# Performance work log

Hardware: AMD Instinct MI355X
Metric: run time of the kernel (lower is better)

The kernel has to match this reference:

```python
import jax, jax.numpy as jnp
import numpy as np

B, S, D = 8, 1024, 1152
H = 16
HD = D // H
HID = int(D * 4.0)
LN_EPS = 1e-5


def layer_norm(x, w, b):
    m = jnp.mean(x, axis=-1, keepdims=True)
    v = jnp.mean(jnp.square(x - m), axis=-1, keepdims=True)
    return (x - m) * jax.lax.rsqrt(v + LN_EPS) * w + b


def modulate(x, shift, scale):
    # shift/scale: [B, D] broadcast over seq
    return x * (1.0 + scale[:, None, :]) + shift[:, None, :]


def setup_inputs() -> dict:
    key = jax.random.key(0)
    ks = jax.random.split(key, 16)
    s = 0.02
    return {
        "x": jax.random.normal(ks[0], (B, S, D), jnp.float32),
        "c": jax.random.normal(ks[1], (B, D), jnp.float32),
        "ln1_w": jnp.ones((D,), jnp.float32),
        "ln1_b": jnp.zeros((D,), jnp.float32),
        "wq": jax.random.normal(ks[2], (D, D), jnp.float32) * s,
        "wk": jax.random.normal(ks[3], (D, D), jnp.float32) * s,
        "wv": jax.random.normal(ks[4], (D, D), jnp.float32) * s,
        "wo": jax.random.normal(ks[5], (D, D), jnp.float32) * s,
        "wo_b": jnp.zeros((D,), jnp.float32),
        "ln2_w": jnp.ones((D,), jnp.float32),
        "ln2_b": jnp.zeros((D,), jnp.float32),
        "fc1_w": jax.random.normal(ks[6], (D, HID), jnp.float32) * s,
        "fc1_b": jnp.zeros((HID,), jnp.float32),
        "fc2_w": jax.random.normal(ks[7], (HID, D), jnp.float32) * s,
        "fc2_b": jnp.zeros((D,), jnp.float32),
        "ada_w": jax.random.normal(ks[8], (D, 6 * D), jnp.float32) * s,
        "ada_b": jnp.zeros((6 * D,), jnp.float32),
    }


def attention(x, wq, wk, wv, wo, wo_b):
    b, s, d = x.shape
    q = (x @ wq).reshape(b, s, H, HD).transpose(0, 2, 1, 3)  # [B,H,S,hd]
    k = (x @ wk).reshape(b, s, H, HD).transpose(0, 2, 1, 3)
    v = (x @ wv).reshape(b, s, H, HD).transpose(0, 2, 1, 3)
    scale = 1.0 / np.sqrt(HD).astype(np.float32)
    att = jnp.einsum("bhqd,bhkd->bhqk", q, k) * scale
    att = jax.nn.softmax(att, axis=-1)
    out = jnp.einsum("bhqk,bhkd->bhqd", att, v)
    out = out.transpose(0, 2, 1, 3).reshape(b, s, d)
    return out @ wo + wo_b


def reference(x, c, ln1_w, ln1_b, wq, wk, wv, wo, wo_b, ln2_w, ln2_b,
              fc1_w, fc1_b, fc2_w, fc2_b, ada_w, ada_b):
    mod = jax.nn.silu(c) @ ada_w + ada_b  # [B, 6D]
    sh_msa, sc_msa, g_msa, sh_mlp, sc_mlp, g_mlp = jnp.split(mod, 6, axis=1)
    h = modulate(layer_norm(x, ln1_w, ln1_b), sh_msa, sc_msa)
    x = x + g_msa[:, None, :] * attention(h, wq, wk, wv, wo, wo_b)
    h = modulate(layer_norm(x, ln2_w, ln2_b), sh_mlp, sc_mlp)
    h = jax.nn.gelu(h @ fc1_w + fc1_b, approximate=False) @ fc2_w + fc2_b
    x = x + g_mlp[:, None, :] * h
    return x
```

## Files before the change

kernel.cpp:

```cpp
#include <hip/hip_runtime.h>
#include <hip/hip_bf16.h>


typedef unsigned short u16;
typedef unsigned int u32;
typedef __attribute__((ext_vector_type(8))) short bf16x8;
typedef __attribute__((ext_vector_type(4))) float f32x4;
typedef __attribute__((ext_vector_type(16))) float f32x16;

#define MFMA16(a, b, c) __builtin_amdgcn_mfma_f32_16x16x32_bf16((a), (b), (c), 0, 0, 0)
#define MFMA32(a, b, c) __builtin_amdgcn_mfma_f32_32x32x16_bf16((a), (b), (c), 0, 0, 0)

__device__ __forceinline__ u16 f2bf(float f) {
  __hip_bfloat16 h = __float2bfloat16(f);
  return __builtin_bit_cast(u16, h);
}

__device__ __forceinline__ float bf2f(u16 u) {
  u32 v = ((u32)u) << 16;
  return __builtin_bit_cast(float, v);
}

__device__ __forceinline__ void gload16(const u16* g, u16* l) {
  __builtin_amdgcn_global_load_lds(
      (const __attribute__((address_space(1))) unsigned int*)(const void*)g,
      (__attribute__((address_space(3))) unsigned int*)(void*)l, 16, 0, 0);
}

__global__ __launch_bounds__(256) void k_modproj1(const float* __restrict__ cc,
                                                  const float* __restrict__ aw,
                                                  float* __restrict__ partial) {
  __shared__ float lc[8][144];
  int kc = blockIdx.y;
  for (int i = threadIdx.x; i < 1152; i += 256) {
    int b = i / 144, k = i % 144;
    float v = cc[b * 1152 + kc * 144 + k];
    lc[b][k] = v / (1.f + __expf(-v));
  }
  __syncthreads();
  int j = blockIdx.x * 256 + threadIdx.x;
  float acc[8] = {0, 0, 0, 0, 0, 0, 0, 0};
  for (int k = 0; k < 144; ++k) {
    float w = aw[(size_t)(kc * 144 + k) * 6912 + j];
    #pragma unroll
    for (int b = 0; b < 8; ++b) acc[b] += lc[b][k] * w;
  }
  #pragma unroll
  for (int b = 0; b < 8; ++b) partial[((size_t)kc * 8 + b) * 6912 + j] = acc[b];
}

__global__ __launch_bounds__(256) void k_modproj2(const float* __restrict__ partial,
                                                  const float* __restrict__ ab,
                                                  float* __restrict__ mo) {
  int j = blockIdx.x * 256 + threadIdx.x;
  float bias = ab[j];
  #pragma unroll
  for (int b = 0; b < 8; ++b) {
    float s = 0.f;
    #pragma unroll
    for (int kc = 0; kc < 8; ++kc) s += partial[((size_t)kc * 8 + b) * 6912 + j];
    mo[(size_t)b * 6912 + j] = s + bias;
  }
}

__global__ __launch_bounds__(256) void k_tcvt(const float* __restrict__ in, u16* __restrict__ out,
                                              int K, int N) {
  __shared__ float t[32][33];
  int tx = threadIdx.x & 31, ty = threadIdx.x >> 5;
  size_t bx = (size_t)blockIdx.x * 32, by = (size_t)blockIdx.y * 32;
  #pragma unroll
  for (int i = 0; i < 4; ++i) t[ty + 8 * i][tx] = in[(by + ty + 8 * i) * N + bx + tx];
  __syncthreads();
  #pragma unroll
  for (int i = 0; i < 4; ++i) out[(bx + ty + 8 * i) * K + by + tx] = f2bf(t[tx][ty + 8 * i]);
}

__global__ __launch_bounds__(256) void k_lnmod(const float* __restrict__ xin,
                                               const float* __restrict__ w,
                                               const float* __restrict__ bs,
                                               const float* __restrict__ mo,
                                               int sh_off, int sc_off, u16* __restrict__ o) {
  int row = blockIdx.x;
  int b = row >> 10;
  int tid = threadIdx.x;
  const float4* x4 = (const float4*)(xin + (size_t)row * 1152);
  float4 v0 = x4[tid];
  float4 v1 = make_float4(0.f, 0.f, 0.f, 0.f);
  if (tid < 32) v1 = x4[256 + tid];
  float s = v0.x + v0.y + v0.z + v0.w + v1.x + v1.y + v1.z + v1.w;
  float sq = v0.x * v0.x + v0.y * v0.y + v0.z * v0.z + v0.w * v0.w +
             v1.x * v1.x + v1.y * v1.y + v1.z * v1.z + v1.w * v1.w;
  #pragma unroll
  for (int d = 32; d > 0; d >>= 1) { s += __shfl_down(s, d); sq += __shfl_down(sq, d); }
  __shared__ float ps[4], pq[4];
  int wid = tid >> 6, lane = tid & 63;
  if (lane == 0) { ps[wid] = s; pq[wid] = sq; }
  __syncthreads();
  float S = ps[0] + ps[1] + ps[2] + ps[3];
  float SQ = pq[0] + pq[1] + pq[2] + pq[3];
  float mean = S * (1.f / 1152.f);
  float var = SQ * (1.f / 1152.f) - mean * mean;
  float rs = rsqrtf(var + 1e-5f);
  const float* shp = mo + (size_t)b * 6912 + sh_off;
  const float* scp = mo + (size_t)b * 6912 + sc_off;
  u16* orow = o + (size_t)row * 1152;
  {
    int col = 4 * tid;
    ushort4 u; float y;
    y = (v0.x - mean) * rs * w[col + 0] + bs[col + 0]; u.x = f2bf(y * (1.f + scp[col + 0]) + shp[col + 0]);
    y = (v0.y - mean) * rs * w[col + 1] + bs[col + 1]; u.y = f2bf(y * (1.f + scp[col + 1]) + shp[col + 1]);
    y = (v0.z - mean) * rs * w[col + 2] + bs[col + 2]; u.z = f2bf(y * (1.f + scp[col + 2]) + shp[col + 2]);
    y = (v0.w - mean) * rs * w[col + 3] + bs[col + 3]; u.w = f2bf(y * (1.f + scp[col + 3]) + shp[col + 3]);
    *(ushort4*)&orow[col] = u;
  }
  if (tid < 32) {
    int col = 1024 + 4 * tid;
    ushort4 u; float y;
    y = (v1.x - mean) * rs * w[col + 0] + bs[col + 0]; u.x = f2bf(y * (1.f + scp[col + 0]) + shp[col + 0]);
    y = (v1.y - mean) * rs * w[col + 1] + bs[col + 1]; u.y = f2bf(y * (1.f + scp[col + 1]) + shp[col + 1]);
    y = (v1.z - mean) * rs * w[col + 2] + bs[col + 2]; u.z = f2bf(y * (1.f + scp[col + 2]) + shp[col + 2]);
    y = (v1.w - mean) * rs * w[col + 3] + bs[col + 3]; u.w = f2bf(y * (1.f + scp[col + 3]) + shp[col + 3]);
    *(ushort4*)&orow[col] = u;
  }
}

template <int EPI>
__global__ __launch_bounds__(512, 2) void k_gemm8(const u16* __restrict__ A,
                                                  const u16* __restrict__ Bt,
                                                  int Kst, int klen,
                                                  u16* __restrict__ Cb,
                                                  const float* __restrict__ bias,
                                                  u16* __restrict__ vt) {
  const int tid = threadIdx.x;
  const int w = tid >> 6, lane = tid & 63;
  const int wm = w >> 2, wn = w & 3;
  const int l31 = lane & 31, hi = lane >> 5;

  const int nwg = gridDim.x * gridDim.y;
  const int id = blockIdx.y * gridDim.x + blockIdx.x;
  const int swz = (id & 7) * (nwg >> 3) + (id >> 3);
  const int tM = (swz / gridDim.x) * 256, tN = (swz % gridDim.x) * 256;
  const int koff = 0;

  __shared__ u16 lA[3][256 * 32];
  __shared__ u16 lB[3][256 * 32];
  f32x16 acc[4][2];
  #pragma unroll
  for (int m = 0; m < 4; ++m)
    #pragma unroll
    for (int n = 0; n < 2; ++n)
      #pragma unroll
      for (int r = 0; r < 16; ++r) acc[m][n][r] = 0.f;

  const int lrow = lane >> 2, lseg = lane & 3;
  const int fl = (lrow & 3) ^ ((lrow >> 2) & 3);
  const u16* gA = A + (size_t)(tM + w * 32 + lrow) * Kst + (lseg ^ fl) * 8 + koff;
  const u16* gB = Bt + (size_t)(tN + w * 32 + lrow) * Kst + (lseg ^ fl) * 8 + koff;
  const size_t rstep = (size_t)16 * Kst;
  const int wo0 = (w * 32) * 32, wo1 = (w * 32 + 16) * 32;
  const int fr = (l31 & 3) ^ ((l31 >> 2) & 3);
  const int c0 = (hi ^ fr) * 8;
  const int c1 = ((hi ^ fr) ^ 2) * 8;
  const int arow = (wm * 128 + l31) * 32;
  const int brow = (wn * 64 + l31) * 32;

#define STAGE(buf, ks)                        \
  do {                                        \
    gload16(gA + (ks), lA[buf] + wo0);        \
    gload16(gA + rstep + (ks), lA[buf] + wo1);\
    gload16(gB + (ks), lB[buf] + wo0);        \
    gload16(gB + rstep + (ks), lB[buf] + wo1);\
  } while (0)

#define COMPUTE(buf)                                                              \
  do {                                                                            \
    bf16x8 af[4][2], bf[2][2];                                                    \
    _Pragma("unroll")                                                             \
    for (int m = 0; m < 4; ++m) {                                                 \
      af[m][0] = *(const bf16x8*)&lA[buf][arow + m * 1024 + c0];                  \
      af[m][1] = *(const bf16x8*)&lA[buf][arow + m * 1024 + c1];                  \
    }                                                                             \
    _Pragma("unroll")                                                             \
    for (int n = 0; n < 2; ++n) {                                                 \
      bf[n][0] = *(const bf16x8*)&lB[buf][brow + n * 1024 + c0];                  \
      bf[n][1] = *(const bf16x8*)&lB[buf][brow + n * 1024 + c1];                  \
    }                                                                             \
    __builtin_amdgcn_s_setprio(1);                                                \
    _Pragma("unroll")                                                             \
    for (int m = 0; m < 4; ++m)                                                   \
      _Pragma("unroll")                                                           \
      for (int n = 0; n < 2; ++n) acc[m][n] = MFMA32(af[m][0], bf[n][0], acc[m][n]); \
    _Pragma("unroll")                                                             \
    for (int m = 0; m < 4; ++m)                                                   \
      _Pragma("unroll")                                                           \
      for (int n = 0; n < 2; ++n) acc[m][n] = MFMA32(af[m][1], bf[n][1], acc[m][n]); \
    __builtin_amdgcn_s_setprio(0);                                                \
  } while (0)

#define WAITBAR(Nst)                                          \
  do {                                                        \
    asm volatile("s_waitcnt vmcnt(" #Nst ")" ::: "memory");   \
    __builtin_amdgcn_s_barrier();                             \
    __builtin_amdgcn_sched_barrier(0);                        \
  } while (0)

  const int nt = klen >> 5;
  STAGE(0, 0);
  STAGE(1, 32);
  int ks = 64;
  for (int g = 0; g < nt / 3 - 1; ++g) {
    WAITBAR(4); STAGE(2, ks);      COMPUTE(0);
    WAITBAR(4); STAGE(0, ks + 32); COMPUTE(1);
    WAITBAR(4); STAGE(1, ks + 64); COMPUTE(2);
    ks += 96;
  }
  WAITBAR(4); STAGE(2, ks); COMPUTE(0);
  WAITBAR(4); COMPUTE(1);
  WAITBAR(0); COMPUTE(2);
#undef STAGE
#undef COMPUTE
#undef WAITBAR

  #pragma unroll
  for (int m = 0; m < 4; ++m)
    #pragma unroll
    for (int n = 0; n < 2; ++n) {
      int gcol = tN + wn * 64 + n * 32 + l31;
      #pragma unroll
      for (int q = 0; q < 4; ++q) {
        int grow0 = tM + wm * 128 + m * 32 + hi * 4 + q * 8;
        if (EPI == 3) {
          if (gcol < 2304) {
            #pragma unroll
            for (int r = 0; r < 4; ++r)
              Cb[(size_t)(grow0 + r) * 3456 + gcol] = f2bf(acc[m][n][q * 4 + r]);
          } else if (gcol < 3456) {
            int qq = gcol - 2304;
            int hh = qq / 72;
            int d = qq - hh * 72;
            int bb = grow0 >> 10, sl = grow0 & 1023;
            ushort4 u;
            u.x = f2bf(acc[m][n][q * 4 + 0]); u.y = f2bf(acc[m][n][q * 4 + 1]);
            u.z = f2bf(acc[m][n][q * 4 + 2]); u.w = f2bf(acc[m][n][q * 4 + 3]);
            *(ushort4*)&vt[(((size_t)bb * 16 + hh) * 72 + d) * 1024 + sl] = u;
          }
        } else {
          const int NC = gridDim.x * 256;
          float bi = bias[gcol];
          #pragma unroll
          for (int r = 0; r < 4; ++r) {
            float z = acc[m][n][q * 4 + r] + bi;
            float z2 = z * z;
            float u = z * __fmaf_rn(z2, -0.0713548162f, -1.5957691216f);
            float e = __expf(u);
            Cb[(size_t)(grow0 + r) * NC + gcol] = f2bf(z * __builtin_amdgcn_rcpf(1.f + e));
          }
        }
      }
    }
}

template <int EPI>
__global__ __launch_bounds__(256) void k_gemm(const u16* __restrict__ A, const u16* __restrict__ Bt,
                                              int Kst, int klen, u16* __restrict__ Cb,
                                              float* __restrict__ Cf,
                                              const float* __restrict__ bias,
                                              const float* __restrict__ res,
                                              const float* __restrict__ mo, int goff,
                                              u16* __restrict__ vt) {
  const int tid = threadIdx.x;
  const int w = tid >> 6, lane = tid & 63;
  const int wr = w >> 1, wc = w & 1;
  const int l31 = lane & 31, hi = lane >> 5;

  const int nwg = gridDim.x * gridDim.y;
  const int id = blockIdx.y * gridDim.x + blockIdx.x;
  const int swz = (id & 7) * (nwg >> 3) + (id >> 3);
  const int tM = (swz / gridDim.x) * 128, tN = (swz % gridDim.x) * 128;
  const int N = gridDim.x * 128;
  const int koff = blockIdx.z * klen;

  __shared__ u16 lA[3][128 * 32];
  __shared__ u16 lB[3][128 * 32];
  f32x16 acc[2][2];
  #pragma unroll
  for (int m = 0; m < 2; ++m)
    #pragma unroll
    for (int n = 0; n < 2; ++n)
      #pragma unroll
      for (int r = 0; r < 16; ++r) acc[m][n][r] = 0.f;

  const int lrow = lane >> 2, lseg = lane & 3;
  const int fl = (lrow & 3) ^ ((lrow >> 2) & 3);
  const u16* gA = A + (size_t)(tM + w * 32 + lrow) * Kst + (lseg ^ fl) * 8 + koff;
  const u16* gB = Bt + (size_t)(tN + w * 32 + lrow) * Kst + (lseg ^ fl) * 8 + koff;
  const size_t rstep = (size_t)16 * Kst;
  const int wo0 = (w * 32) * 32, wo1 = (w * 32 + 16) * 32;
  const int fr = (l31 & 3) ^ ((l31 >> 2) & 3);
  const int c0 = (hi ^ fr) * 8;
  const int c1 = ((hi ^ fr) ^ 2) * 8;
  const int arow = (wr * 64 + l31) * 32;
  const int brow = (wc * 64 + l31) * 32;

#define STAGE(buf, ks)                        \
  do {                                        \
    gload16(gA + (ks), lA[buf] + wo0);        \
    gload16(gA + rstep + (ks), lA[buf] + wo1);\
    gload16(gB + (ks), lB[buf] + wo0);        \
    gload16(gB + rstep + (ks), lB[buf] + wo1);\
  } while (0)

#define COMPUTE(buf)                                                            \
  do {                                                                          \
    bf16x8 a00 = *(const bf16x8*)&lA[buf][arow + c0];                           \
    bf16x8 a01 = *(const bf16x8*)&lA[buf][arow + c1];                           \
    bf16x8 a10 = *(const bf16x8*)&lA[buf][arow + 1024 + c0];                    \
    bf16x8 a11 = *(const bf16x8*)&lA[buf][arow + 1024 + c1];                    \
    bf16x8 b00 = *(const bf16x8*)&lB[buf][brow + c0];                           \
    bf16x8 b01 = *(const bf16x8*)&lB[buf][brow + c1];                           \
    bf16x8 b10 = *(const bf16x8*)&lB[buf][brow + 1024 + c0];                    \
    bf16x8 b11 = *(const bf16x8*)&lB[buf][brow + 1024 + c1];                    \
    __builtin_amdgcn_s_setprio(1);                                              \
    acc[0][0] = MFMA32(a00, b00, acc[0][0]);                                    \
    acc[0][1] = MFMA32(a00, b10, acc[0][1]);                                    \
    acc[1][0] = MFMA32(a10, b00, acc[1][0]);                                    \
    acc[1][1] = MFMA32(a10, b10, acc[1][1]);                                    \
    acc[0][0] = MFMA32(a01, b01, acc[0][0]);                                    \
    acc[0][1] = MFMA32(a01, b11, acc[0][1]);                                    \
    acc[1][0] = MFMA32(a11, b01, acc[1][0]);                                    \
    acc[1][1] = MFMA32(a11, b11, acc[1][1]);                                    \
    __builtin_amdgcn_s_setprio(0);                                              \
  } while (0)

#define WAITBAR(Nst)                                          \
  do {                                                        \
    asm volatile("s_waitcnt vmcnt(" #Nst ")" ::: "memory");   \
    __builtin_amdgcn_s_barrier();                             \
    __builtin_amdgcn_sched_barrier(0);                        \
  } while (0)

  const int nt = klen >> 5;
  STAGE(0, 0);
  STAGE(1, 32);
  int ks = 64;
  for (int g = 0; g < nt / 3 - 1; ++g) {
    WAITBAR(4); STAGE(2, ks);      COMPUTE(0);
    WAITBAR(4); STAGE(0, ks + 32); COMPUTE(1);
    WAITBAR(4); STAGE(1, ks + 64); COMPUTE(2);
    ks += 96;
  }
  WAITBAR(4); STAGE(2, ks); COMPUTE(0);
  WAITBAR(4); COMPUTE(1);
  WAITBAR(0); COMPUTE(2);
#undef STAGE
#undef COMPUTE
#undef WAITBAR

  #pragma unroll
  for (int m = 0; m < 2; ++m)
    #pragma unroll
    for (int n = 0; n < 2; ++n) {
      int gcol = tN + wc * 64 + n * 32 + l31;
      #pragma unroll
      for (int q = 0; q < 4; ++q) {
        int grow0 = tM + wr * 64 + m * 32 + hi * 4 + q * 8;
        if (EPI == 5) {
          u16* Po = Cb + (size_t)blockIdx.z * ((size_t)gridDim.y * 128) * N;
          #pragma unroll
          for (int r = 0; r < 4; ++r)
            Po[(size_t)(grow0 + r) * N + gcol] = f2bf(acc[m][n][q * 4 + r]);
        } else {
          float g = mo[(size_t)(grow0 >> 10) * 6912 + goff + gcol];
          float bi = bias[gcol];
          #pragma unroll
          for (int r = 0; r < 4; ++r) {
            size_t idx = (size_t)(grow0 + r) * N + gcol;
            Cf[idx] = res[idx] + g * (acc[m][n][q * 4 + r] + bi);
          }
        }
      }
    }
}

__global__ __launch_bounds__(256) void k_fc2red(const u16* __restrict__ p,
                                                const float* __restrict__ x1,
                                                const float* __restrict__ bias,
                                                const float* __restrict__ mo,
                                                float* __restrict__ out) {
  size_t i = ((size_t)blockIdx.x * 256 + threadIdx.x) * 4;
  int row = (int)(i / 1152);
  int col = (int)(i - (size_t)row * 1152);
  int b = row >> 10;
  ushort4 a0 = *(const ushort4*)(p + i);
  ushort4 a1 = *(const ushort4*)(p + 9437184ull + i);
  float4 r = *(const float4*)(x1 + i);
  const float* gp = mo + (size_t)b * 6912 + 5760 + col;
  const float* bp = bias + col;
  float4 o;
  o.x = r.x + gp[0] * (bf2f(a0.x) + bf2f(a1.x) + bp[0]);
  o.y = r.y + gp[1] * (bf2f(a0.y) + bf2f(a1.y) + bp[1]);
  o.z = r.z + gp[2] * (bf2f(a0.z) + bf2f(a1.z) + bp[2]);
  o.w = r.w + gp[3] * (bf2f(a0.w) + bf2f(a1.w) + bp[3]);
  *(float4*)(out + i) = o;
}

__global__ __launch_bounds__(256) void k_attn(const u16* __restrict__ QKV, const u16* __restrict__ Vt,
                                              u16* __restrict__ O) {
  const int tid = threadIdx.x;
  const int w = tid >> 6, lane = tid & 63;
  const int lr = lane & 15, kg = lane >> 4;
  int bx = blockIdx.x;
  bx = (bx & 7) * 256 + (bx >> 3);
  const int qt = bx & 15, h = (bx >> 4) & 15, b = bx >> 8;

  __shared__ u16 lQ[64][104];
  __shared__ u16 lK[64][104];
  __shared__ u16 lVt[80][72];
  __shared__ u16 lPt[4][16][72];

  const size_t qkbase = (size_t)b * 1024 * 3456 + (size_t)h * 72;
  const u16* Qg = QKV + qkbase;
  const u16* Kg = QKV + qkbase + 1152;
  const u16* Vg = Vt + ((size_t)(b * 16 + h) * 72) * 1024;

  const uint4 z4 = make_uint4(0, 0, 0, 0);
  for (int L = tid; L < 192; L += 256) {
    int r = L / 3, s = L - (L / 3) * 3;
    *(uint4*)&lQ[r][72 + s * 8] = z4;
    *(uint4*)&lK[r][72 + s * 8] = z4;
  }
  for (int L = tid; L < 72; L += 256) {
    int r = L / 9, s = L - (L / 9) * 9;
    *(uint4*)&lVt[72 + r][s * 8] = z4;
  }
  {
    int L = tid; int r = L / 9, s = L - r * 9;
    *(uint4*)&lQ[r][s * 8] = *(const uint4*)(Qg + (size_t)(qt * 64 + r) * 3456 + s * 8);
    L = tid + 256; r = L / 9; s = L - r * 9;
    *(uint4*)&lQ[r][s * 8] = *(const uint4*)(Qg + (size_t)(qt * 64 + r) * 3456 + s * 8);
    if (tid < 64) {
      L = tid + 512; r = L / 9; s = L - r * 9;
      *(uint4*)&lQ[r][s * 8] = *(const uint4*)(Qg + (size_t)(qt * 64 + r) * 3456 + s * 8);
    }
  }
  __syncthreads();

  bf16x8 bq[3];
  #pragma unroll
  for (int ks = 0; ks < 3; ++ks) bq[ks] = *(const bf16x8*)&lQ[w * 16 + lr][ks * 32 + kg * 8];

  const float scale = 0.11785113019775793f;
  float mrun = -1e30f, lrun = 0.f;
  f32x4 oacc[5];
  #pragma unroll
  for (int nd = 0; nd < 5; ++nd) oacc[nd] = f32x4{0.f, 0.f, 0.f, 0.f};

  for (int kt = 0; kt < 16; ++kt) {
    __syncthreads();
    {
      int L = tid; int r = L / 9, s = L - (L / 9) * 9;
      *(uint4*)&lK[r][s * 8] = *(const uint4*)(Kg + (size_t)(kt * 64 + r) * 3456 + s * 8);
      int d = tid >> 3, sg = tid & 7;
      *(uint4*)&lVt[d][sg * 8] = *(const uint4*)(Vg + (size_t)d * 1024 + kt * 64 + sg * 8);
      L = tid + 256; r = L / 9; s = L - r * 9;
      *(uint4*)&lK[r][s * 8] = *(const uint4*)(Kg + (size_t)(kt * 64 + r) * 3456 + s * 8);
      d = (tid + 256) >> 3; sg = tid & 7;
      *(uint4*)&lVt[d][sg * 8] = *(const uint4*)(Vg + (size_t)d * 1024 + kt * 64 + sg * 8);
      if (tid < 64) {
        L = tid + 512; r = L / 9; s = L - r * 9;
        *(uint4*)&lK[r][s * 8] = *(const uint4*)(Kg + (size_t)(kt * 64 + r) * 3456 + s * 8);
        d = (tid + 512) >> 3;
        *(uint4*)&lVt[d][sg * 8] = *(const uint4*)(Vg + (size_t)d * 1024 + kt * 64 + sg * 8);
      }
    }
    __syncthreads();

    f32x4 sfr[4];
    __builtin_amdgcn_s_setprio(1);
    #pragma unroll
    for (int kb = 0; kb < 4; ++kb) {
      f32x4 sv = f32x4{0.f, 0.f, 0.f, 0.f};
      #pragma unroll
      for (int ks = 0; ks < 3; ++ks) {
        bf16x8 ak = *(const bf16x8*)&lK[kb * 16 + lr][ks * 32 + kg * 8];
        sv = MFMA16(ak, bq[ks], sv);
      }
      sfr[kb] = sv;
    }
    __builtin_amdgcn_s_setprio(0);

    float mx = sfr[0][0];
    #pragma unroll
    for (int kb = 0; kb < 4; ++kb)
      #pragma unroll
      for (int r = 0; r < 4; ++r) mx = fmaxf(mx, sfr[kb][r]);
    mx = fmaxf(mx, __shfl_xor(mx, 16));
    mx = fmaxf(mx, __shfl_xor(mx, 32));
    mx *= scale;
    float mn = fmaxf(mrun, mx);
    float al = __expf(mrun - mn);
    mrun = mn;
    float sum = 0.f;
    #pragma unroll
    for (int kb = 0; kb < 4; ++kb) {
      #pragma unroll
      for (int rp = 0; rp < 2; ++rp) {
        float p0 = __expf(__fmaf_rn(sfr[kb][2 * rp], scale, -mn));
        float p1 = __expf(__fmaf_rn(sfr[kb][2 * rp + 1], scale, -mn));
        sum += p0 + p1;
        u32 pk = (u32)f2bf(p0) | ((u32)f2bf(p1) << 16);
        *(u32*)&lPt[w][lr][kb * 16 + kg * 4 + rp * 2] = pk;
      }
    }
    sum += __shfl_xor(sum, 16);
    sum += __shfl_xor(sum, 32);
    lrun = lrun * al + sum;
    #pragma unroll
    for (int nd = 0; nd < 5; ++nd)
      #pragma unroll
      for (int r = 0; r < 4; ++r) oacc[nd][r] *= al;

    __builtin_amdgcn_s_setprio(1);
    #pragma unroll
    for (int s = 0; s < 2; ++s) {
      bf16x8 bp = *(const bf16x8*)&lPt[w][lr][s * 32 + kg * 8];
      #pragma unroll
      for (int nd = 0; nd < 5; ++nd) {
        bf16x8 av = *(const bf16x8*)&lVt[nd * 16 + lr][s * 32 + kg * 8];
        oacc[nd] = MFMA16(av, bp, oacc[nd]);
      }
    }
    __builtin_amdgcn_s_setprio(0);
  }

  float inv = 1.f / lrun;
  size_t orow = ((size_t)b * 1024 + qt * 64 + w * 16 + lr) * 1152 + h * 72;
  #pragma unroll
  for (int nd = 0; nd < 5; ++nd) {
    int d0 = nd * 16 + kg * 4;
    if (d0 < 72) {
      ushort4 u;
      u.x = f2bf(oacc[nd][0] * inv);
      u.y = f2bf(oacc[nd][1] * inv);
      u.z = f2bf(oacc[nd][2] * inv);
      u.w = f2bf(oacc[nd][3] * inv);
      *(ushort4*)&O[orow + d0] = u;
    }
  }
}

extern "C" void kernel_launch(void* const* d_in, const int* in_sizes, int n_in,
                              void* d_out, int out_size, void* d_ws, size_t ws_size,
                              hipStream_t stream) {
  const float* x     = (const float*)d_in[0];
  const float* c     = (const float*)d_in[1];
  const float* ln1_w = (const float*)d_in[2];
  const float* ln1_b = (const float*)d_in[3];
  const float* wq    = (const float*)d_in[4];
  const float* wk    = (const float*)d_in[5];
  const float* wv    = (const float*)d_in[6];
  const float* wo    = (const float*)d_in[7];
  const float* wo_b  = (const float*)d_in[8];
  const float* ln2_w = (const float*)d_in[9];
  const float* ln2_b = (const float*)d_in[10];
  const float* fc1_w = (const float*)d_in[11];
  const float* fc1_b = (const float*)d_in[12];
  const float* fc2_w = (const float*)d_in[13];
  const float* fc2_b = (const float*)d_in[14];
  const float* ada_w = (const float*)d_in[15];
  const float* ada_b = (const float*)d_in[16];
  float* out = (float*)d_out;

  char* base = (char*)d_ws;
  size_t off = 0;
  auto alloc = [&](size_t nbytes) -> void* {
    void* p = base + off;
    off += (nbytes + 255) & ~(size_t)255;
    return p;
  };
  const size_t MD = 8192ull * 1152;
  float* partial = (float*)alloc(64ull * 6912 * 4);
  float* modb   = (float*)alloc(55296 * 4);
  u16* qkvT = (u16*)alloc(3584ull * 1152 * 2);
  u16* woT  = (u16*)alloc(1152ull * 1152 * 2);
  u16* fc1T = (u16*)alloc(4608ull * 1152 * 2);
  u16* fc2T = (u16*)alloc(1152ull * 4608 * 2);
  u16* hbuf = (u16*)alloc(MD * 2);
  float* x1 = (float*)alloc(MD * 4);
  u16* vtb  = (u16*)alloc(128ull * 72 * 1024 * 2);
  u16* fc2p = (u16*)alloc(2ull * MD * 2);
  u16* big  = (u16*)alloc(8192ull * 4608 * 2);
  u16* qkv = big;
  u16* m1 = big;

  k_modproj1<<<dim3(27, 8), 256, 0, stream>>>(c, ada_w, partial);
  k_modproj2<<<27, 256, 0, stream>>>(partial, ada_b, modb);
  k_tcvt<<<dim3(36, 36), 256, 0, stream>>>(wq, qkvT, 1152, 1152);
  k_tcvt<<<dim3(36, 36), 256, 0, stream>>>(wk, qkvT + 1152ull * 1152, 1152, 1152);
  k_tcvt<<<dim3(36, 36), 256, 0, stream>>>(wv, qkvT + 2304ull * 1152, 1152, 1152);
  k_tcvt<<<dim3(36, 36), 256, 0, stream>>>(wo, woT, 1152, 1152);
  k_tcvt<<<dim3(144, 36), 256, 0, stream>>>(fc1_w, fc1T, 1152, 4608);
  k_tcvt<<<dim3(36, 144), 256, 0, stream>>>(fc2_w, fc2T, 4608, 1152);

  k_lnmod<<<8192, 256, 0, stream>>>(x, ln1_w, ln1_b, modb, 0, 1152, hbuf);
  k_gemm8<3><<<dim3(14, 32), 512, 0, stream>>>(hbuf, qkvT, 1152, 1152, qkv, nullptr, vtb);
  k_attn<<<2048, 256, 0, stream>>>(qkv, vtb, hbuf);
  k_gemm<1><<<dim3(9, 64), 256, 0, stream>>>(hbuf, woT, 1152, 1152, nullptr, x1, wo_b, x, modb, 2304, nullptr);
  k_lnmod<<<8192, 256, 0, stream>>>(x1, ln2_w, ln2_b, modb, 3456, 4608, hbuf);
  k_gemm8<2><<<dim3(18, 32), 512, 0, stream>>>(hbuf, fc1T, 1152, 1152, m1, fc1_b, nullptr);
  k_gemm<5><<<dim3(9, 64, 2), 256, 0, stream>>>(m1, fc2T, 4608, 2304, fc2p, nullptr, nullptr, nullptr, nullptr, 0, nullptr);
  k_fc2red<<<9216, 256, 0, stream>>>(fc2p, x1, fc2_b, modb, out);
}
```

Baseline: 577.3 us.

## Restructure 256x256 GEMM main loop into finer-grained ping-pong phases

Replaces the triple-buffered K-loop of the 8-wave GEMM with a 2x2 LDS buffer layout. Each 32-wide K slice is split into two phases of eight MFMAs, and each phase issues a half-stage (A or B) of the next global-to-LDS loads. This interleaves loads with compute more finely and keeps fewer fragments live per phase, aiming to hide memory latency better. In exchange there are more barriers per K step, and the loop requires klen to be a multiple of 128, which holds for 1152.

```diff
diff --git a/kernel.cpp b/kernel.cpp
--- a/kernel.cpp
+++ b/kernel.cpp
@@ -125,12 +125,12 @@
 }
 
 template <int EPI>
-__global__ __launch_bounds__(512, 2) void k_gemm8(const u16* __restrict__ A,
-                                                  const u16* __restrict__ Bt,
-                                                  int Kst, int klen,
-                                                  u16* __restrict__ Cb,
-                                                  const float* __restrict__ bias,
-                                                  u16* __restrict__ vt) {
+__global__ __launch_bounds__(512, 2) void k_gemm8p(const u16* __restrict__ A,
+                                                   const u16* __restrict__ Bt,
+                                                   int Kst, int klen,
+                                                   u16* __restrict__ Cb,
+                                                   const float* __restrict__ bias,
+                                                   u16* __restrict__ vt) {
   const int tid = threadIdx.x;
   const int w = tid >> 6, lane = tid & 63;
   const int wm = w >> 2, wn = w & 3;
@@ -140,10 +140,9 @@
   const int id = blockIdx.y * gridDim.x + blockIdx.x;
   const int swz = (id & 7) * (nwg >> 3) + (id >> 3);
   const int tM = (swz / gridDim.x) * 256, tN = (swz % gridDim.x) * 256;
-  const int koff = 0;
-
-  __shared__ u16 lA[3][256 * 32];
-  __shared__ u16 lB[3][256 * 32];
+
+  __shared__ u16 lA[2][2][256 * 32];
+  __shared__ u16 lB[2][2][256 * 32];
   f32x16 acc[4][2];
   #pragma unroll
   for (int m = 0; m < 4; ++m)
@@ -154,8 +153,8 @@
 
   const int lrow = lane >> 2, lseg = lane & 3;
   const int fl = (lrow & 3) ^ ((lrow >> 2) & 3);
-  const u16* gA = A + (size_t)(tM + w * 32 + lrow) * Kst + (lseg ^ fl) * 8 + koff;
-  const u16* gB = Bt + (size_t)(tN + w * 32 + lrow) * Kst + (lseg ^ fl) * 8 + koff;
+  const u16* gA = A + (size_t)(tM + w * 32 + lrow) * Kst + (lseg ^ fl) * 8;
+  const u16* gB = Bt + (size_t)(tN + w * 32 + lrow) * Kst + (lseg ^ fl) * 8;
   const size_t rstep = (size_t)16 * Kst;
   const int wo0 = (w * 32) * 32, wo1 = (w * 32 + 16) * 32;
   const int fr = (l31 & 3) ^ ((l31 >> 2) & 3);
@@ -164,62 +163,73 @@
   const int arow = (wm * 128 + l31) * 32;
   const int brow = (wn * 64 + l31) * 32;
 
-#define STAGE(buf, ks)                        \
-  do {                                        \
-    gload16(gA + (ks), lA[buf] + wo0);        \
-    gload16(gA + rstep + (ks), lA[buf] + wo1);\
-    gload16(gB + (ks), lB[buf] + wo0);        \
-    gload16(gB + rstep + (ks), lB[buf] + wo1);\
+#define SA(BUF, KH, KO)                                       \
+  do {                                                        \
+    gload16(gA + (KO), &lA[BUF][KH][wo0]);                    \
+    gload16(gA + rstep + (KO), &lA[BUF][KH][wo1]);            \
   } while (0)
-
-#define COMPUTE(buf)                                                              \
-  do {                                                                            \
-    bf16x8 af[4][2], bf[2][2];                                                    \
-    _Pragma("unroll")                                                             \
-    for (int m = 0; m < 4; ++m) {                                                 \
-      af[m][0] = *(const bf16x8*)&lA[buf][arow + m * 1024 + c0];                  \
-      af[m][1] = *(const bf16x8*)&lA[buf][arow + m * 1024 + c1];                  \
-    }                                                                             \
-    _Pragma("unroll")                                                             \
-    for (int n = 0; n < 2; ++n) {                                                 \
-      bf[n][0] = *(const bf16x8*)&lB[buf][brow + n * 1024 + c0];                  \
-      bf[n][1] = *(const bf16x8*)&lB[buf][brow + n * 1024 + c1];                  \
-    }                                                                             \
-    __builtin_amdgcn_s_setprio(1);                                                \
-    _Pragma("unroll")                                                             \
-    for (int m = 0; m < 4; ++m)                                                   \
-      _Pragma("unroll")                                                           \
-      for (int n = 0; n < 2; ++n) acc[m][n] = MFMA32(af[m][0], bf[n][0], acc[m][n]); \
-    _Pragma("unroll")                                                             \
-    for (int m = 0; m < 4; ++m)                                                   \
-      _Pragma("unroll")                                                           \
-      for (int n = 0; n < 2; ++n) acc[m][n] = MFMA32(af[m][1], bf[n][1], acc[m][n]); \
-    __builtin_amdgcn_s_setprio(0);                                                \
+#define SB(BUF, KH, KO)                                       \
+  do {                                                        \
+    gload16(gB + (KO), &lB[BUF][KH][wo0]);                    \
+    gload16(gB + rstep + (KO), &lB[BUF][KH][wo1]);            \
   } while (0)
-
-#define WAITBAR(Nst)                                          \
-  do {                                                        \
-    asm volatile("s_waitcnt vmcnt(" #Nst ")" ::: "memory");   \
-    __builtin_amdgcn_s_barrier();                             \
-    __builtin_amdgcn_sched_barrier(0);                        \
+#define VM(Nst) asm volatile("s_waitcnt vmcnt(" #Nst ")" ::: "memory")
+
+#define PHASE(CB, KH, PM, STAGE_STMT)                                            \
+  do {                                                                           \
+    __builtin_amdgcn_s_barrier();                                                \
+    __builtin_amdgcn_sched_barrier(0);                                           \
+    bf16x8 a0_ = *(const bf16x8*)&lA[CB][KH][arow + (2 * (PM)) * 1024 + c0];     \
+    bf16x8 a1_ = *(const bf16x8*)&lA[CB][KH][arow + (2 * (PM)) * 1024 + c1];     \
+    bf16x8 a2_ = *(const bf16x8*)&lA[CB][KH][arow + (2 * (PM) + 1) * 1024 + c0]; \
+    bf16x8 a3_ = *(const bf16x8*)&lA[CB][KH][arow + (2 * (PM) + 1) * 1024 + c1]; \
+    bf16x8 b0_ = *(const bf16x8*)&lB[CB][KH][brow + c0];                         \
+    bf16x8 b1_ = *(const bf16x8*)&lB[CB][KH][brow + c1];                         \
+    bf16x8 b2_ = *(const bf16x8*)&lB[CB][KH][brow + 1024 + c0];                  \
+    bf16x8 b3_ = *(const bf16x8*)&lB[CB][KH][brow + 1024 + c1];                  \
+    STAGE_STMT;                                                                  \
+    asm volatile("s_waitcnt lgkmcnt(0)" ::: "memory");                           \
+    __builtin_amdgcn_sched_barrier(0);                                           \
+    __builtin_amdgcn_s_setprio(1);                                               \
+    acc[2 * (PM)][0]     = MFMA32(a0_, b0_, acc[2 * (PM)][0]);                   \
+    acc[2 * (PM)][1]     = MFMA32(a0_, b2_, acc[2 * (PM)][1]);                   \
+    acc[2 * (PM) + 1][0] = MFMA32(a2_, b0_, acc[2 * (PM) + 1][0]);               \
+    acc[2 * (PM) + 1][1] = MFMA32(a2_, b2_, acc[2 * (PM) + 1][1]);               \
+    acc[2 * (PM)][0]     = MFMA32(a1_, b1_, acc[2 * (PM)][0]);                   \
+    acc[2 * (PM)][1]     = MFMA32(a1_, b3_, acc[2 * (PM)][1]);                   \
+    acc[2 * (PM) + 1][0] = MFMA32(a3_, b1_, acc[2 * (PM) + 1][0]);               \
+    acc[2 * (PM) + 1][1] = MFMA32(a3_, b3_, acc[2 * (PM) + 1][1]);               \
+    __builtin_amdgcn_s_setprio(0);                                               \
   } while (0)
 
-  const int nt = klen >> 5;
-  STAGE(0, 0);
-  STAGE(1, 32);
-  int ks = 64;
-  for (int g = 0; g < nt / 3 - 1; ++g) {
-    WAITBAR(4); STAGE(2, ks);      COMPUTE(0);
-    WAITBAR(4); STAGE(0, ks + 32); COMPUTE(1);
-    WAITBAR(4); STAGE(1, ks + 64); COMPUTE(2);
-    ks += 96;
-  }
-  WAITBAR(4); STAGE(2, ks); COMPUTE(0);
-  WAITBAR(4); COMPUTE(1);
-  WAITBAR(0); COMPUTE(2);
-#undef STAGE
-#undef COMPUTE
-#undef WAITBAR
+  const int NIT = klen >> 7;
+  SA(0, 0, 0); SB(0, 0, 0); SA(0, 1, 32); SB(0, 1, 32); SA(1, 0, 64);
+  for (int it = 0; it < NIT - 1; ++it) {
+    const int kb = it * 128;
+    VM(6); PHASE(0, 0, 0, SB(1, 0, kb + 64));
+           PHASE(0, 0, 1, SA(1, 1, kb + 96));
+    VM(6); PHASE(0, 1, 0, SB(1, 1, kb + 96));
+           PHASE(0, 1, 1, SA(0, 0, kb + 128));
+    VM(6); PHASE(1, 0, 0, SB(0, 0, kb + 128));
+           PHASE(1, 0, 1, SA(0, 1, kb + 160));
+    VM(6); PHASE(1, 1, 0, SB(0, 1, kb + 160));
+           PHASE(1, 1, 1, SA(1, 0, kb + 192));
+  }
+  {
+    const int kb = (NIT - 1) * 128;
+    VM(6); PHASE(0, 0, 0, SB(1, 0, kb + 64));
+           PHASE(0, 0, 1, SA(1, 1, kb + 96));
+    VM(6); PHASE(0, 1, 0, SB(1, 1, kb + 96));
+           PHASE(0, 1, 1, (void)0);
+    VM(4); PHASE(1, 0, 0, (void)0);
+           PHASE(1, 0, 1, (void)0);
+    VM(0); PHASE(1, 1, 0, (void)0);
+           PHASE(1, 1, 1, (void)0);
+  }
+#undef SA
+#undef SB
+#undef VM
+#undef PHASE
 
   #pragma unroll
   for (int m = 0; m < 4; ++m)
@@ -603,11 +613,11 @@
   k_tcvt<<<dim3(36, 144), 256, 0, stream>>>(fc2_w, fc2T, 4608, 1152);
 
   k_lnmod<<<8192, 256, 0, stream>>>(x, ln1_w, ln1_b, modb, 0, 1152, hbuf);
-  k_gemm8<3><<<dim3(14, 32), 512, 0, stream>>>(hbuf, qkvT, 1152, 1152, qkv, nullptr, vtb);
+  k_gemm8p<3><<<dim3(14, 32), 512, 0, stream>>>(hbuf, qkvT, 1152, 1152, qkv, nullptr, vtb);
   k_attn<<<2048, 256, 0, stream>>>(qkv, vtb, hbuf);
   k_gemm<1><<<dim3(9, 64), 256, 0, stream>>>(hbuf, woT, 1152, 1152, nullptr, x1, wo_b, x, modb, 2304, nullptr);
   k_lnmod<<<8192, 256, 0, stream>>>(x1, ln2_w, ln2_b, modb, 3456, 4608, hbuf);
-  k_gemm8<2><<<dim3(18, 32), 512, 0, stream>>>(hbuf, fc1T, 1152, 1152, m1, fc1_b, nullptr);
+  k_gemm8p<2><<<dim3(18, 32), 512, 0, stream>>>(hbuf, fc1T, 1152, 1152, m1, fc1_b, nullptr);
   k_gemm<5><<<dim3(9, 64, 2), 256, 0, stream>>>(m1, fc2T, 4608, 2304, fc2p, nullptr, nullptr, nullptr, nullptr, 0, nullptr);
   k_fc2red<<<9216, 256, 0, stream>>>(fc2p, x1, fc2_b, modb, out);
 }
```

Measured after the change: 565.7 us. -2.0%, faster.
